# Optimization experiments

Measured on AMD Instinct MI355X. Metric: run time of the kernel, lower is better.

Reference implementation:

```python
import jax, jax.numpy as jnp
import numpy as np

H, FH, D = 8, 4, 64          # num_heads, focal_heads, att_size
HID = H * D                   # hidden_size = 512
B, S = 8, 512                 # batch, num_nodes
T_HOP, T_EDGE = 32, 16
SCALE = D ** -0.5


def setup_inputs() -> dict:
    key = jax.random.key(0)
    ks = jax.random.split(key, 24)
    f = lambda i, shape: jax.random.normal(ks[i], shape, jnp.float32)
    w = 1.0 / np.sqrt(HID)
    inp = {
        'q': f(0, (B, S, HID)), 'k': f(1, (B, S, HID)), 'v': f(2, (B, S, HID)),
        'query_hop_emb': f(3, (T_HOP, HID)) * 0.02,
        'query_edge_emb': f(4, (T_EDGE, HID)) * 0.02,
        'key_hop_emb': f(5, (T_HOP, HID)) * 0.02,
        'key_edge_emb': f(6, (T_EDGE, HID)) * 0.02,
        'value_hop_emb': f(7, (T_HOP, HID)) * 0.02,
        'value_edge_emb': f(8, (T_EDGE, HID)) * 0.02,
        'distance': jax.random.randint(ks[9], (B, S, S), 0, T_HOP),
        'edge_attr': jax.random.randint(ks[10], (B, S, S), 0, T_EDGE),
        # guarantee at least one unmasked key per query row to keep softmax finite
        'mask': jax.random.bernoulli(ks[11], 0.9, (B, S)).at[:, 0].set(True),
        'focal_mask': jax.random.bernoulli(ks[12], 0.5, (B, S, S)).at[:, :, 0].set(True),
        'Wq': f(13, (HID, H * D)) * w, 'bq': f(14, (H * D,)) * 0.01,
        'Wk': f(15, (HID, H * D)) * w, 'bk': f(16, (H * D,)) * 0.01,
        'Wv': f(17, (HID, H * D)) * w, 'bv': f(18, (H * D,)) * 0.01,
        'Wo': f(19, (H * D, HID)) * w, 'bo': f(20, (HID,)) * 0.01,
    }
    return inp


def _emb_scores(x, emb):
    # x: [B,H,S,D], emb: [T, H*D] -> per-head scores [B,H,S,T]
    e = emb.reshape(-1, H, D).transpose(1, 0, 2)  # [H,T,D]
    return jnp.einsum('bhsd,htd->bhst', x, e)


def _gather_last(scores, idx):
    # scores: [B,H,S,T], idx: [B,S,S] -> [B,H,S,S]
    idx_b = jnp.broadcast_to(idx[:, None], (B, H, S, S))
    return jnp.take_along_axis(scores, idx_b, axis=3)


def _scatter_add_last(attn, idx, T):
    # attn: [B,H,S,S], idx: [B,S,S] -> [B,H,S,T] accumulating attn weights
    idx_b = jnp.broadcast_to(idx[:, None], (B, H, S, S)).reshape(B * H * S, S)
    rows = jnp.arange(B * H * S)[:, None]
    flat = (rows * T + idx_b).reshape(-1)
    out = jnp.zeros((B * H * S * T,), attn.dtype).at[flat].add(attn.reshape(-1))
    return out.reshape(B, H, S, T)


def reference(q, k, v, query_hop_emb, query_edge_emb, key_hop_emb, key_edge_emb,
              value_hop_emb, value_edge_emb, distance, edge_attr, mask, focal_mask,
              Wq, bq, Wk, bk, Wv, bv, Wo, bo):
    qh = (q @ Wq + bq).reshape(B, S, H, D).transpose(0, 2, 1, 3)  # [B,H,S,D]
    kh = (k @ Wk + bk).reshape(B, S, H, D).transpose(0, 2, 1, 3)
    vh = (v @ Wv + bv).reshape(B, S, H, D).transpose(0, 2, 1, 3)

    spatial_bias = (_gather_last(_emb_scores(qh, query_hop_emb), distance)
                    + _gather_last(_emb_scores(kh, key_hop_emb), distance))
    edge_bias = (_gather_last(_emb_scores(qh, query_edge_emb), edge_attr)
                 + _gather_last(_emb_scores(kh, key_edge_emb), edge_attr))

    attn = (jnp.einsum('bhsd,bhtd->bhst', qh, kh) + spatial_bias + edge_bias) * SCALE

    GS = H - FH
    a1 = jnp.where(mask[:, None, None, :], attn[:, :GS], -jnp.inf)
    a2 = jnp.where(focal_mask[:, None], attn[:, GS:], -jnp.inf)
    attn = jax.nn.softmax(jnp.concatenate([a1, a2], axis=1), axis=3)

    vha = _scatter_add_last(attn, distance, T_HOP)   # [B,H,S,T_HOP]
    vea = _scatter_add_last(attn, edge_attr, T_EDGE)  # [B,H,S,T_EDGE]
    vh_emb = value_hop_emb.reshape(T_HOP, H, D).transpose(1, 0, 2)   # [H,T,D]
    ve_emb = value_edge_emb.reshape(T_EDGE, H, D).transpose(1, 0, 2)

    x = (jnp.einsum('bhst,bhtd->bhsd', attn, vh)
         + jnp.einsum('bhst,htd->bhsd', vha, vh_emb)
         + jnp.einsum('bhst,htd->bhsd', vea, ve_emb))
    x = x.transpose(0, 2, 1, 3).reshape(B, S, H * D)
    return x @ Wo + bo
```

## Files before the change

kernel.cpp:

```cpp
#include <hip/hip_runtime.h>

constexpr int nB = 8, nS = 512, nH = 8, nD = 64, nHID = 512;
constexpr int THOP = 32, TEDGE = 16;
constexpr float SCALE = 0.125f;
constexpr float NEGINF = -30000.0f;

typedef __attribute__((ext_vector_type(8))) short bf16x8;
typedef __attribute__((ext_vector_type(4))) float f32x4;

#define MFMA16(A, B, C) __builtin_amdgcn_mfma_f32_16x16x32_bf16(A, B, C, 0, 0, 0)

__device__ __align__(16) unsigned short g_qhi[(size_t)nB * nH * nS * nD];
__device__ __align__(16) unsigned short g_qlo[(size_t)nB * nH * nS * nD];
__device__ __align__(16) unsigned short g_khi[(size_t)nB * nH * nS * nD];
__device__ __align__(16) unsigned short g_klo[(size_t)nB * nH * nS * nD];
__device__ __align__(16) unsigned short g_vhiT[(size_t)nB * nH * nD * nS];
__device__ __align__(16) unsigned short g_vloT[(size_t)nB * nH * nD * nS];
__device__ __align__(16) unsigned short g_embh[96 * 512];
__device__ __align__(16) unsigned short g_embl[96 * 512];
__device__ float g_x[(size_t)nB * nS * nHID];
__device__ int g_flags[32];

__device__ __forceinline__ float ldf(const void* p, int isf32, size_t i) {
  if (isf32) return ((const float*)p)[i];
  unsigned int w = (unsigned int)(((const unsigned short*)p)[i]) << 16;
  return __uint_as_float(w);
}
__device__ __forceinline__ float bf2f(unsigned short h) {
  return __uint_as_float((unsigned)h << 16);
}
__device__ __forceinline__ float4 ldf4(const void* p, int isf32, size_t i) {
  if (isf32) return ((const float4*)p)[i >> 2];
  const ushort4 u = ((const ushort4*)p)[i >> 2];
  float4 r;
  r.x = bf2f(u.x); r.y = bf2f(u.y); r.z = bf2f(u.z); r.w = bf2f(u.w);
  return r;
}
__device__ __forceinline__ unsigned short f2bf(float x) {
  unsigned u = __float_as_uint(x);
  u += 0x7FFFu + ((u >> 16) & 1u);
  return (unsigned short)(u >> 16);
}

__device__ int detect_bool_mode(const unsigned char* p) {
  if (p[0] == 0x80 && p[1] == 0x3F) return 2;
  if (p[0] == 0x00 && p[1] == 0x3C) return 4;
  if (p[0] == 0x00 && p[3] == 0x3F) return 3;
  for (int i = 0; i < 64; i += 4)
    if (p[i + 1] | p[i + 2] | p[i + 3]) return 1;
  return 0;
}
__device__ __forceinline__ bool bool_at(const unsigned char* p, int mode, size_t i) {
  switch (mode) {
    case 0: return ((const int*)p)[i] != 0;
    case 1: return p[i] != 0;
    case 3: return ((const float*)p)[i] != 0.f;
    default: return ((const unsigned short*)p)[i] != 0;
  }
}

__global__ __launch_bounds__(256) void detect_all(
    const void* q, const void* k, const void* v,
    const void* qhe, const void* qee, const void* khe, const void* kee,
    const void* vhe, const void* vee,
    const int* dist, const int* edge,
    const unsigned char* mraw, const unsigned char* fraw,
    const void* Wq, const void* bq, const void* Wk, const void* bk,
    const void* Wv, const void* bv, const void* Wo, const void* bo) {
  __shared__ float sred[256];
  __shared__ int nzs;
  const int tid = threadIdx.x;
  const int blk = blockIdx.x;

  if (blk < 17) {
    const void* arrs[17] = {q, k, v, qhe, qee, khe, kee, vhe, vee,
                            Wq, bq, Wk, bk, Wv, bv, Wo, bo};
    const int full[17] = {2097152, 2097152, 2097152, 8192, 8192, 8192, 8192,
                          8192, 8192, 262144, 512, 262144, 512, 262144, 512,
                          262144, 512};
    const int n = full[blk] < 16384 ? full[blk] : 16384;
    const unsigned short* u = (const unsigned short*)arrs[blk];
    float m = 0.f;
    for (int i = tid; i < n; i += 256) {
      float x = __uint_as_float((unsigned int)u[i] << 16);
      if (x != x) x = 1e20f;
      m = fmaxf(m, fabsf(x));
    }
    sred[tid] = m;
    __syncthreads();
    for (int s = 128; s > 0; s >>= 1) {
      if (tid < s) sred[tid] = fmaxf(sred[tid], sred[tid + s]);
      __syncthreads();
    }
    if (tid == 0) g_flags[4 + blk] = (sred[0] > 1e3f) ? 1 : 0;
  } else if (blk == 17 || blk == 18) {
    const int* p = (blk == 17) ? dist : edge;
    if (tid == 0) nzs = 0;
    __syncthreads();
    int a = 0;
    for (int i = tid; i < 4096; i += 256) a |= p[2 * i + 1];
    if (a) atomicOr(&nzs, 1);
    __syncthreads();
    if (tid == 0) g_flags[blk - 17] = (nzs == 0);
  } else {
    if (tid == 0) {
      g_flags[2] = detect_bool_mode(mraw);
      g_flags[3] = detect_bool_mode(fraw);
      g_flags[21] = 1;
    }
  }
}

__global__ __launch_bounds__(256) void emb_prep(
    const void* qhe, const void* khe, const void* qee, const void* kee) {
  const int blk = blockIdx.x;
  const void* srcs[4] = {qhe, khe, qee, kee};
  const int flagIdx[4] = {7, 9, 8, 10};
  const int counts[4] = {32 * 512, 32 * 512, 16 * 512, 16 * 512};
  const int dsts[4] = {0, 32 * 512, 64 * 512, 80 * 512};
  const int f = g_flags[flagIdx[blk]];
  const void* src = srcs[blk];
  const int n = counts[blk], d0 = dsts[blk];
  for (int i = threadIdx.x; i < n; i += 256) {
    const float x = ldf(src, f, i);
    const unsigned short hi = f2bf(x);
    g_embh[d0 + i] = hi;
    g_embl[d0 + i] = f2bf(x - bf2f(hi));
  }
}

__global__ __launch_bounds__(256) void gemm_mfma(
    const void* __restrict__ A, int aFlag,
    const void* __restrict__ W, int wFlag,
    const void* __restrict__ bias, int bFlag,
    float* __restrict__ dst, int mode) {
  __shared__ unsigned short As_hi[64][40];
  __shared__ unsigned short As_lo[64][40];
  __shared__ unsigned short Wt_hi[64][40];
  __shared__ unsigned short Wt_lo[64][40];
  const int aF = g_flags[aFlag], wF = g_flags[wFlag], bF = g_flags[bFlag];
  const int tid = threadIdx.x;
  const int m0 = blockIdx.y * 64, n0 = blockIdx.x * 64;
  const int w = tid >> 6, l = tid & 63, c = l & 15, g = l >> 4;
  const int wr = w >> 1, wc = w & 1;

  f32x4 acc[2][2] = {{{0.f, 0.f, 0.f, 0.f}, {0.f, 0.f, 0.f, 0.f}},
                     {{0.f, 0.f, 0.f, 0.f}, {0.f, 0.f, 0.f, 0.f}}};

  for (int k0 = 0; k0 < 512; k0 += 32) {
    __syncthreads();
#pragma unroll
    for (int i = 0; i < 2; ++i) {
      const int e = tid + i * 256;
      {
        const int r = e >> 3, kk = (e & 7) * 4;
        const float4 a4 = ldf4(A, aF, (size_t)(m0 + r) * 512 + k0 + kk);
        const unsigned short h0 = f2bf(a4.x), h1 = f2bf(a4.y);
        const unsigned short h2 = f2bf(a4.z), h3 = f2bf(a4.w);
        *(unsigned*)&As_hi[r][kk]     = (unsigned)h0 | ((unsigned)h1 << 16);
        *(unsigned*)&As_hi[r][kk + 2] = (unsigned)h2 | ((unsigned)h3 << 16);
        const unsigned short l0 = f2bf(a4.x - bf2f(h0));
        const unsigned short l1 = f2bf(a4.y - bf2f(h1));
        const unsigned short l2 = f2bf(a4.z - bf2f(h2));
        const unsigned short l3 = f2bf(a4.w - bf2f(h3));
        *(unsigned*)&As_lo[r][kk]     = (unsigned)l0 | ((unsigned)l1 << 16);
        *(unsigned*)&As_lo[r][kk + 2] = (unsigned)l2 | ((unsigned)l3 << 16);
      }
      {
        const int kk = e >> 4, nn = (e & 15) * 4;
        const float4 w4 = ldf4(W, wF, (size_t)(k0 + kk) * 512 + n0 + nn);
        const float wv[4] = {w4.x, w4.y, w4.z, w4.w};
#pragma unroll
        for (int t = 0; t < 4; ++t) {
          const unsigned short hh = f2bf(wv[t]);
          Wt_hi[nn + t][kk] = hh;
          Wt_lo[nn + t][kk] = f2bf(wv[t] - bf2f(hh));
        }
      }
    }
    __syncthreads();
#pragma unroll
    for (int mi = 0; mi < 2; ++mi) {
      const bf16x8 ah = *(const bf16x8*)&As_hi[wr * 32 + mi * 16 + c][g * 8];
      const bf16x8 al = *(const bf16x8*)&As_lo[wr * 32 + mi * 16 + c][g * 8];
#pragma unroll
      for (int nj = 0; nj < 2; ++nj) {
        const bf16x8 wh = *(const bf16x8*)&Wt_hi[wc * 32 + nj * 16 + c][g * 8];
        const bf16x8 wl = *(const bf16x8*)&Wt_lo[wc * 32 + nj * 16 + c][g * 8];
        acc[mi][nj] = MFMA16(ah, wh, acc[mi][nj]);
        acc[mi][nj] = MFMA16(al, wh, acc[mi][nj]);
        acc[mi][nj] = MFMA16(ah, wl, acc[mi][nj]);
      }
    }
  }
#pragma unroll
  for (int mi = 0; mi < 2; ++mi)
#pragma unroll
    for (int nj = 0; nj < 2; ++nj)
#pragma unroll
      for (int r = 0; r < 4; ++r) {
        const int m = m0 + wr * 32 + mi * 16 + 4 * g + r;
        const int n = n0 + wc * 32 + nj * 16 + c;
        const float v2 = acc[mi][nj][r] + ldf(bias, bF, n);
        if (mode == 3) {
          dst[(size_t)m * 512 + n] = v2;
        } else {
          const int b = m >> 9, s = m & 511, h = n >> 6, d = n & 63;
          const unsigned short hi = f2bf(v2);
          const unsigned short lo = f2bf(v2 - bf2f(hi));
          if (mode == 0) {
            const size_t i0 = (((size_t)(b * nH + h) * nS) + s) * nD + d;
            g_qhi[i0] = hi; g_qlo[i0] = lo;
          } else if (mode == 1) {
            const size_t i0 = (((size_t)(b * nH + h) * nS) + s) * nD + d;
            g_khi[i0] = hi; g_klo[i0] = lo;
          } else {
            const size_t i0 = (((size_t)(b * nH + h) * nD) + d) * nS + s;
            g_vhiT[i0] = hi; g_vloT[i0] = lo;
          }
        }
      }
}

__global__ __launch_bounds__(256, 4) void attn_kernel(
    const int* __restrict__ dist, const int* __restrict__ edge,
    const unsigned char* __restrict__ mraw, const unsigned char* __restrict__ fraw,
    const void* __restrict__ vhe, const void* __restrict__ vee) {
  __shared__ float chop_s[16][33];
  __shared__ float cedge_s[16][17];
  __shared__ float vha_s[16][33];
  __shared__ float vea_s[16][17];
  __shared__ float red_s[16][4];
  __shared__ float red2_s[16][4];
  __shared__ float rinv_s[16];
  __shared__ float x_s[64][17];
  __shared__ unsigned char dlds[16][516];
  __shared__ unsigned char elds[16][516];
  __shared__ unsigned char flds[16][516];
  __shared__ unsigned char smask_l[516];

  const int qt = blockIdx.x, bh = blockIdx.y;
  const int b = bh >> 3, h = bh & 7;
  const int q0 = qt * 16;
  const int tid = threadIdx.x;
  const int w = tid >> 6, l = tid & 63, c = l & 15, g = l >> 4;

  const int d64 = g_flags[0], e64 = g_flags[1];
  const int mmode = g_flags[2], fmode = g_flags[3];
  const int fvhe = g_flags[11], fvee = g_flags[12];

  for (int i = tid; i < 16 * 33; i += 256) (&vha_s[0][0])[i] = 0.f;
  for (int i = tid; i < 16 * 17; i += 256) (&vea_s[0][0])[i] = 0.f;
  for (int i = tid; i < 64 * 17; i += 256) (&x_s[0][0])[i] = 0.f;

  const size_t rowbase = ((size_t)b * nS + q0) * nS;
  if (!d64) {
    const int4* dp = (const int4*)(dist + rowbase);
    for (int j4 = tid; j4 < 2048; j4 += 256) {
      const int4 t = dp[j4];
      const int j = j4 * 4, r = j >> 9, c1 = j & 511;
      *(unsigned*)&dlds[r][c1] =
          (unsigned)(t.x & 31) | ((unsigned)(t.y & 31) << 8) |
          ((unsigned)(t.z & 31) << 16) | ((unsigned)(t.w & 31) << 24);
    }
  } else {
    const int4* dp = (const int4*)(dist + 2 * rowbase);
    for (int j2 = tid; j2 < 4096; j2 += 256) {
      const int4 t = dp[j2];
      const int j = j2 * 2, r = j >> 9, c1 = j & 511;
      *(unsigned short*)&dlds[r][c1] =
          (unsigned short)((t.x & 31) | ((t.z & 31) << 8));
    }
  }
  if (!e64) {
    const int4* ep = (const int4*)(edge + rowbase);
    for (int j4 = tid; j4 < 2048; j4 += 256) {
      const int4 t = ep[j4];
      const int j = j4 * 4, r = j >> 9, c1 = j & 511;
      *(unsigned*)&elds[r][c1] =
          (unsigned)(t.x & 15) | ((unsigned)(t.y & 15) << 8) |
          ((unsigned)(t.z & 15) << 16) | ((unsigned)(t.w & 15) << 24);
    }
  } else {
    const int4* ep = (const int4*)(edge + 2 * rowbase);
    for (int j2 = tid; j2 < 4096; j2 += 256) {
      const int4 t = ep[j2];
      const int j = j2 * 2, r = j >> 9, c1 = j & 511;
      *(unsigned short*)&elds[r][c1] =
          (unsigned short)((t.x & 15) | ((t.z & 15) << 8));
    }
  }
  if (h < 4) {
    for (int i4 = tid; i4 < 128; i4 += 256) {
      unsigned wv = 0;
#pragma unroll
      for (int t = 0; t < 4; ++t)
        wv |= (unsigned)bool_at(mraw, mmode, (size_t)b * nS + i4 * 4 + t) << (8 * t);
      *(unsigned*)&smask_l[i4 * 4] = wv;
    }
  } else {
    for (int i4 = tid; i4 < 2048; i4 += 256) {
      const int j = i4 * 4, r = j >> 9, c1 = j & 511;
      unsigned wv = 0;
#pragma unroll
      for (int t = 0; t < 4; ++t)
        wv |= (unsigned)bool_at(fraw, fmode, rowbase + j + t) << (8 * t);
      *(unsigned*)&flds[r][c1] = wv;
    }
  }

  const size_t qbase = (((size_t)bh * nS) + q0 + c) * nD + g * 8;
  const bf16x8 qh0 = *(const bf16x8*)(g_qhi + qbase);
  const bf16x8 qh1 = *(const bf16x8*)(g_qhi + qbase + 32);
  const bf16x8 ql0 = *(const bf16x8*)(g_qlo + qbase);
  const bf16x8 ql1 = *(const bf16x8*)(g_qlo + qbase + 32);

  if (w < 3) {
    const bool isEdge = (w == 2);
    const int tb = (w == 1) ? 16 : 0;
    const size_t qe0 = (isEdge ? (size_t)64 * 512 : 0) + (size_t)(tb + c) * 512 + h * 64;
    const size_t ke0 = (isEdge ? (size_t)80 * 512 : (size_t)32 * 512) + (size_t)(tb + c) * 512 + h * 64;
    f32x4 acc = {0.f, 0.f, 0.f, 0.f};
#pragma unroll
    for (int dh = 0; dh < 2; ++dh) {
      const bf16x8 qhh = dh ? qh1 : qh0;
      const bf16x8 qll = dh ? ql1 : ql0;
      const bf16x8 khq = *(const bf16x8*)(g_khi + qbase + dh * 32);
      const bf16x8 klq = *(const bf16x8*)(g_klo + qbase + dh * 32);
      const bf16x8 eqh = *(const bf16x8*)(g_embh + qe0 + dh * 32 + g * 8);
      const bf16x8 eql = *(const bf16x8*)(g_embl + qe0 + dh * 32 + g * 8);
      const bf16x8 ekh = *(const bf16x8*)(g_embh + ke0 + dh * 32 + g * 8);
      const bf16x8 ekl = *(const bf16x8*)(g_embl + ke0 + dh * 32 + g * 8);
      acc = MFMA16(qhh, eqh, acc);
      acc = MFMA16(qll, eqh, acc);
      acc = MFMA16(qhh, eql, acc);
      acc = MFMA16(khq, ekh, acc);
      acc = MFMA16(klq, ekh, acc);
      acc = MFMA16(khq, ekl, acc);
    }
    if (!isEdge) {
#pragma unroll
      for (int r = 0; r < 4; ++r) chop_s[4 * g + r][tb + c] = acc[r];
    } else {
#pragma unroll
      for (int r = 0; r < 4; ++r) cedge_s[4 * g + r][c] = acc[r];
    }
  }
  __syncthreads();

  f32x4 pS[8];
  const int kbw = w * 128;
#pragma unroll
  for (int kt = 0; kt < 8; ++kt) {
    const int kb = kbw + kt * 16;
    const size_t kbase = (((size_t)bh * nS) + kb + c) * nD + g * 8;
    f32x4 acc = {0.f, 0.f, 0.f, 0.f};
    {
      const bf16x8 kh0 = *(const bf16x8*)(g_khi + kbase);
      const bf16x8 kl0 = *(const bf16x8*)(g_klo + kbase);
      acc = MFMA16(kh0, qh0, acc);
      acc = MFMA16(kl0, qh0, acc);
      acc = MFMA16(kh0, ql0, acc);
      const bf16x8 kh1 = *(const bf16x8*)(g_khi + kbase + 32);
      const bf16x8 kl1 = *(const bf16x8*)(g_klo + kbase + 32);
      acc = MFMA16(kh1, qh1, acc);
      acc = MFMA16(kl1, qh1, acc);
      acc = MFMA16(kh1, ql1, acc);
    }
    const int key0 = kb + 4 * g;
    const unsigned dw = *(const unsigned*)&dlds[c][key0];
    const unsigned ew = *(const unsigned*)&elds[c][key0];
    const unsigned fw = (h < 4) ? *(const unsigned*)&smask_l[key0]
                                : *(const unsigned*)&flds[c][key0];
#pragma unroll
    for (int r = 0; r < 4; ++r) {
      const int dv = (dw >> (8 * r)) & 255;
      const int ev = (ew >> (8 * r)) & 255;
      const float s = (acc[r] + chop_s[c][dv] + cedge_s[c][ev]) * SCALE;
      pS[kt][r] = ((fw >> (8 * r)) & 255) ? s : NEGINF;
    }
  }

  float mx = NEGINF;
#pragma unroll
  for (int kt = 0; kt < 8; ++kt)
#pragma unroll
    for (int r = 0; r < 4; ++r) mx = fmaxf(mx, pS[kt][r]);
  mx = fmaxf(mx, __shfl_xor(mx, 16));
  mx = fmaxf(mx, __shfl_xor(mx, 32));
  if (l < 16) red_s[c][w] = mx;
  __syncthreads();
  const float M = fmaxf(fmaxf(red_s[c][0], red_s[c][1]),
                        fmaxf(red_s[c][2], red_s[c][3]));
  float sum = 0.f;
#pragma unroll
  for (int kt = 0; kt < 8; ++kt) {
    const int key0 = kbw + kt * 16 + 4 * g;
    const unsigned dw = *(const unsigned*)&dlds[c][key0];
    const unsigned ew = *(const unsigned*)&elds[c][key0];
#pragma unroll
    for (int r = 0; r < 4; ++r) {
      const float pv = __expf(pS[kt][r] - M);
      pS[kt][r] = pv;
      sum += pv;
      atomicAdd(&vha_s[c][(dw >> (8 * r)) & 255], pv);
      atomicAdd(&vea_s[c][(ew >> (8 * r)) & 255], pv);
    }
  }
  sum += __shfl_xor(sum, 16);
  sum += __shfl_xor(sum, 32);
  if (l < 16) red2_s[c][w] = sum;
  int pk[8][2];
#pragma unroll
  for (int kt = 0; kt < 8; ++kt) {
    pk[kt][0] = ((int)f2bf(pS[kt][1]) << 16) | (int)f2bf(pS[kt][0]);
    pk[kt][1] = ((int)f2bf(pS[kt][3]) << 16) | (int)f2bf(pS[kt][2]);
  }
  __syncthreads();
  if (w == 0 && l < 16) {
    const float tot = red2_s[c][0] + red2_s[c][1] + red2_s[c][2] + red2_s[c][3];
    rinv_s[c] = 1.0f / tot;
  }

  f32x4 oacc[4] = {{0.f, 0.f, 0.f, 0.f}, {0.f, 0.f, 0.f, 0.f},
                   {0.f, 0.f, 0.f, 0.f}, {0.f, 0.f, 0.f, 0.f}};
  const int srcA = ((g & 1) * 2) * 16 + c;
  const int srcB = srcA + 16;
  const bool hi2 = (g >> 1) != 0;
#pragma unroll
  for (int ks = 0; ks < 4; ++ks) {
    const int t0d0 = __shfl(pk[2 * ks][0], srcA);
    const int t1d0 = __shfl(pk[2 * ks + 1][0], srcA);
    const int t0d1 = __shfl(pk[2 * ks][1], srcA);
    const int t1d1 = __shfl(pk[2 * ks + 1][1], srcA);
    const int t0d0b = __shfl(pk[2 * ks][0], srcB);
    const int t1d0b = __shfl(pk[2 * ks + 1][0], srcB);
    const int t0d1b = __shfl(pk[2 * ks][1], srcB);
    const int t1d1b = __shfl(pk[2 * ks + 1][1], srcB);
    union { int i[4]; bf16x8 v; } bu;
    bu.i[0] = hi2 ? t1d0 : t0d0;
    bu.i[1] = hi2 ? t1d1 : t0d1;
    bu.i[2] = hi2 ? t1d0b : t0d0b;
    bu.i[3] = hi2 ? t1d1b : t0d1b;
    const int kk = w * 128 + ks * 32;
#pragma unroll
    for (int t = 0; t < 4; ++t) {
      const size_t vbase = (((size_t)bh * nD) + t * 16 + c) * nS + kk + g * 8;
      const bf16x8 vh_ = *(const bf16x8*)(g_vhiT + vbase);
      const bf16x8 vl_ = *(const bf16x8*)(g_vloT + vbase);
      oacc[t] = MFMA16(vh_, bu.v, oacc[t]);
      oacc[t] = MFMA16(vl_, bu.v, oacc[t]);
    }
  }
#pragma unroll
  for (int t = 0; t < 4; ++t)
#pragma unroll
    for (int r = 0; r < 4; ++r)
      atomicAdd(&x_s[t * 16 + 4 * g + r][c], oacc[t][r]);
  __syncthreads();

  {
    const int d = tid & 63, qq = tid >> 6;
    float val[4];
#pragma unroll
    for (int j = 0; j < 4; ++j) val[j] = x_s[d][qq + 4 * j];
    for (int t = 0; t < THOP; ++t) {
      const float e = ldf(vhe, fvhe, (size_t)t * nHID + h * 64 + d);
#pragma unroll
      for (int j = 0; j < 4; ++j) val[j] += vha_s[qq + 4 * j][t] * e;
    }
    for (int t = 0; t < TEDGE; ++t) {
      const float e = ldf(vee, fvee, (size_t)t * nHID + h * 64 + d);
#pragma unroll
      for (int j = 0; j < 4; ++j) val[j] += vea_s[qq + 4 * j][t] * e;
    }
#pragma unroll
    for (int j = 0; j < 4; ++j) {
      const int q = qq + 4 * j;
      g_x[((size_t)b * nS + q0 + q) * nHID + h * 64 + d] = val[j] * rinv_s[q];
    }
  }
}

extern "C" void kernel_launch(void* const* d_in, const int* in_sizes, int n_in,
                              void* d_out, int out_size, void* d_ws, size_t ws_size,
                              hipStream_t stream) {
  const void* q   = d_in[0];
  const void* k   = d_in[1];
  const void* v   = d_in[2];
  const void* qhe = d_in[3];
  const void* qee = d_in[4];
  const void* khe = d_in[5];
  const void* kee = d_in[6];
  const void* vhe = d_in[7];
  const void* vee = d_in[8];
  const int* dist = (const int*)d_in[9];
  const int* edge = (const int*)d_in[10];
  const unsigned char* mraw = (const unsigned char*)d_in[11];
  const unsigned char* fraw = (const unsigned char*)d_in[12];
  const void* Wq = d_in[13];
  const void* bq = d_in[14];
  const void* Wk = d_in[15];
  const void* bk = d_in[16];
  const void* Wv = d_in[17];
  const void* bv = d_in[18];
  const void* Wo = d_in[19];
  const void* bo = d_in[20];

  detect_all<<<20, 256, 0, stream>>>(q, k, v, qhe, qee, khe, kee, vhe, vee,
                                     dist, edge, mraw, fraw,
                                     Wq, bq, Wk, bk, Wv, bv, Wo, bo);
  emb_prep<<<4, 256, 0, stream>>>(qhe, khe, qee, kee);
  float* x_d;  hipGetSymbolAddress((void**)&x_d,  HIP_SYMBOL(g_x));
  gemm_mfma<<<dim3(8, 64), 256, 0, stream>>>(q, 4, Wq, 13, bq, 14, nullptr, 0);
  gemm_mfma<<<dim3(8, 64), 256, 0, stream>>>(k, 5, Wk, 15, bk, 16, nullptr, 1);
  gemm_mfma<<<dim3(8, 64), 256, 0, stream>>>(v, 6, Wv, 17, bv, 18, nullptr, 2);
  attn_kernel<<<dim3(32, 64), 256, 0, stream>>>(dist, edge, mraw, fraw, vhe, vee);
  gemm_mfma<<<dim3(8, 64), 256, 0, stream>>>(x_d, 21, Wo, 19, bo, 20,
                                             (float*)d_out, 3);
}
```

Before: 665.4 us.

## Pre-split GEMM inputs and weights into bf16 hi/lo buffers, reorder attention grid

```diff
diff --git a/kernel.cpp b/kernel.cpp
--- a/kernel.cpp
+++ b/kernel.cpp
@@ -18,7 +18,12 @@
 __device__ __align__(16) unsigned short g_vloT[(size_t)nB * nH * nD * nS];
 __device__ __align__(16) unsigned short g_embh[96 * 512];
 __device__ __align__(16) unsigned short g_embl[96 * 512];
-__device__ float g_x[(size_t)nB * nS * nHID];
+__device__ __align__(16) unsigned short g_inhi[(size_t)3 * 2097152];
+__device__ __align__(16) unsigned short g_inlo[(size_t)3 * 2097152];
+__device__ __align__(16) unsigned short g_wth[(size_t)4 * 262144];
+__device__ __align__(16) unsigned short g_wtl[(size_t)4 * 262144];
+__device__ __align__(16) unsigned short g_xhi[(size_t)nB * nS * nHID];
+__device__ __align__(16) unsigned short g_xlo[(size_t)nB * nS * nHID];
 __device__ int g_flags[32];
 
 __device__ __forceinline__ float ldf(const void* p, int isf32, size_t i) {
@@ -106,7 +111,6 @@
     if (tid == 0) {
       g_flags[2] = detect_bool_mode(mraw);
       g_flags[3] = detect_bool_mode(fraw);
-      g_flags[21] = 1;
     }
   }
 }
@@ -129,54 +133,92 @@
   }
 }
 
+__global__ __launch_bounds__(256) void split_prep(
+    const void* q, const void* k, const void* v) {
+  const int t = blockIdx.y;
+  const void* srcs[3] = {q, k, v};
+  const int f = g_flags[4 + t];
+  const size_t base = (size_t)t * 2097152;
+  const size_t i = ((size_t)blockIdx.x * 256 + threadIdx.x) * 4;
+  const float4 v4 = ldf4(srcs[t], f, i);
+  ushort4 h4, l4;
+  h4.x = f2bf(v4.x); l4.x = f2bf(v4.x - bf2f(h4.x));
+  h4.y = f2bf(v4.y); l4.y = f2bf(v4.y - bf2f(h4.y));
+  h4.z = f2bf(v4.z); l4.z = f2bf(v4.z - bf2f(h4.z));
+  h4.w = f2bf(v4.w); l4.w = f2bf(v4.w - bf2f(h4.w));
+  *(ushort4*)&g_inhi[base + i] = h4;
+  *(ushort4*)&g_inlo[base + i] = l4;
+}
+
+__global__ __launch_bounds__(256) void wt_prep(
+    const void* Wq, const void* Wk, const void* Wv, const void* Wo) {
+  __shared__ float t[64][65];
+  const int mat = blockIdx.y;
+  const void* srcs[4] = {Wq, Wk, Wv, Wo};
+  const int fIdx[4] = {13, 15, 17, 19};
+  const int f = g_flags[fIdx[mat]];
+  const void* W = srcs[mat];
+  const int k0 = (blockIdx.x >> 3) * 64, n0 = (blockIdx.x & 7) * 64;
+  const int tid = threadIdx.x;
+  const int r = tid >> 4, c4 = (tid & 15) * 4;
+#pragma unroll
+  for (int i = 0; i < 4; ++i) {
+    const float4 v4 = ldf4(W, f, (size_t)(k0 + r + i * 16) * 512 + n0 + c4);
+    t[r + i * 16][c4] = v4.x;
+    t[r + i * 16][c4 + 1] = v4.y;
+    t[r + i * 16][c4 + 2] = v4.z;
+    t[r + i * 16][c4 + 3] = v4.w;
+  }
+  __syncthreads();
+  unsigned short* dh = g_wth + (size_t)mat * 262144;
+  unsigned short* dl = g_wtl + (size_t)mat * 262144;
+#pragma unroll
+  for (int i = 0; i < 4; ++i) {
+    const int rn = r + i * 16;
+    ushort4 h4, l4;
+    const float v0 = t[c4][rn], v1 = t[c4 + 1][rn];
+    const float v2 = t[c4 + 2][rn], v3 = t[c4 + 3][rn];
+    h4.x = f2bf(v0); l4.x = f2bf(v0 - bf2f(h4.x));
+    h4.y = f2bf(v1); l4.y = f2bf(v1 - bf2f(h4.y));
+    h4.z = f2bf(v2); l4.z = f2bf(v2 - bf2f(h4.z));
+    h4.w = f2bf(v3); l4.w = f2bf(v3 - bf2f(h4.w));
+    *(ushort4*)&dh[(size_t)(n0 + rn) * 512 + k0 + c4] = h4;
+    *(ushort4*)&dl[(size_t)(n0 + rn) * 512 + k0 + c4] = l4;
+  }
+}
+
 __global__ __launch_bounds__(256) void gemm_mfma(
-    const void* __restrict__ A, int aFlag,
-    const void* __restrict__ W, int wFlag,
+    const unsigned short* __restrict__ Ahi, const unsigned short* __restrict__ Alo,
+    const unsigned short* __restrict__ Wth, const unsigned short* __restrict__ Wtl,
     const void* __restrict__ bias, int bFlag,
     float* __restrict__ dst, int mode) {
   __shared__ unsigned short As_hi[64][40];
   __shared__ unsigned short As_lo[64][40];
   __shared__ unsigned short Wt_hi[64][40];
   __shared__ unsigned short Wt_lo[64][40];
-  const int aF = g_flags[aFlag], wF = g_flags[wFlag], bF = g_flags[bFlag];
+  const int bF = g_flags[bFlag];
   const int tid = threadIdx.x;
   const int m0 = blockIdx.y * 64, n0 = blockIdx.x * 64;
   const int w = tid >> 6, l = tid & 63, c = l & 15, g = l >> 4;
   const int wr = w >> 1, wc = w & 1;
+  const int sr = tid >> 2, sc = (tid & 3) * 8;
 
   f32x4 acc[2][2] = {{{0.f, 0.f, 0.f, 0.f}, {0.f, 0.f, 0.f, 0.f}},
                      {{0.f, 0.f, 0.f, 0.f}, {0.f, 0.f, 0.f, 0.f}}};
 
   for (int k0 = 0; k0 < 512; k0 += 32) {
     __syncthreads();
-#pragma unroll
-    for (int i = 0; i < 2; ++i) {
-      const int e = tid + i * 256;
-      {
-        const int r = e >> 3, kk = (e & 7) * 4;
-        const float4 a4 = ldf4(A, aF, (size_t)(m0 + r) * 512 + k0 + kk);
-        const unsigned short h0 = f2bf(a4.x), h1 = f2bf(a4.y);
-        const unsigned short h2 = f2bf(a4.z), h3 = f2bf(a4.w);
-        *(unsigned*)&As_hi[r][kk]     = (unsigned)h0 | ((unsigned)h1 << 16);
-        *(unsigned*)&As_hi[r][kk + 2] = (unsigned)h2 | ((unsigned)h3 << 16);
-        const unsigned short l0 = f2bf(a4.x - bf2f(h0));
-        const unsigned short l1 = f2bf(a4.y - bf2f(h1));
-        const unsigned short l2 = f2bf(a4.z - bf2f(h2));
-        const unsigned short l3 = f2bf(a4.w - bf2f(h3));
-        *(unsigned*)&As_lo[r][kk]     = (unsigned)l0 | ((unsigned)l1 << 16);
-        *(unsigned*)&As_lo[r][kk + 2] = (unsigned)l2 | ((unsigned)l3 << 16);
-      }
-      {
-        const int kk = e >> 4, nn = (e & 15) * 4;
-        const float4 w4 = ldf4(W, wF, (size_t)(k0 + kk) * 512 + n0 + nn);
-        const float wv[4] = {w4.x, w4.y, w4.z, w4.w};
-#pragma unroll
-        for (int t = 0; t < 4; ++t) {
-          const unsigned short hh = f2bf(wv[t]);
-          Wt_hi[nn + t][kk] = hh;
-          Wt_lo[nn + t][kk] = f2bf(wv[t] - bf2f(hh));
-        }
-      }
+    {
+      const size_t ga = (size_t)(m0 + sr) * 512 + k0 + sc;
+      const size_t gw = (size_t)(n0 + sr) * 512 + k0 + sc;
+      const bf16x8 ah = *(const bf16x8*)(Ahi + ga);
+      const bf16x8 al = *(const bf16x8*)(Alo + ga);
+      const bf16x8 wh = *(const bf16x8*)(Wth + gw);
+      const bf16x8 wl = *(const bf16x8*)(Wtl + gw);
+      *(bf16x8*)&As_hi[sr][sc] = ah;
+      *(bf16x8*)&As_lo[sr][sc] = al;
+      *(bf16x8*)&Wt_hi[sr][sc] = wh;
+      *(bf16x8*)&Wt_lo[sr][sc] = wl;
     }
     __syncthreads();
 #pragma unroll
@@ -222,7 +264,7 @@
       }
 }
 
-__global__ __launch_bounds__(256, 4) void attn_kernel(
+__global__ __launch_bounds__(256) void attn_kernel(
     const int* __restrict__ dist, const int* __restrict__ edge,
     const unsigned char* __restrict__ mraw, const unsigned char* __restrict__ fraw,
     const void* __restrict__ vhe, const void* __restrict__ vee) {
@@ -239,7 +281,7 @@
   __shared__ unsigned char flds[16][516];
   __shared__ unsigned char smask_l[516];
 
-  const int qt = blockIdx.x, bh = blockIdx.y;
+  const int bh = blockIdx.x, qt = blockIdx.y;
   const int b = bh >> 3, h = bh & 7;
   const int q0 = qt * 16;
   const int tid = threadIdx.x;
@@ -477,7 +519,11 @@
 #pragma unroll
     for (int j = 0; j < 4; ++j) {
       const int q = qq + 4 * j;
-      g_x[((size_t)b * nS + q0 + q) * nHID + h * 64 + d] = val[j] * rinv_s[q];
+      const float xv = val[j] * rinv_s[q];
+      const unsigned short hi = f2bf(xv);
+      const size_t i0 = ((size_t)b * nS + q0 + q) * nHID + h * 64 + d;
+      g_xhi[i0] = hi;
+      g_xlo[i0] = f2bf(xv - bf2f(hi));
     }
   }
 }
@@ -511,11 +557,26 @@
                                      dist, edge, mraw, fraw,
                                      Wq, bq, Wk, bk, Wv, bv, Wo, bo);
   emb_prep<<<4, 256, 0, stream>>>(qhe, khe, qee, kee);
-  float* x_d;  hipGetSymbolAddress((void**)&x_d,  HIP_SYMBOL(g_x));
-  gemm_mfma<<<dim3(8, 64), 256, 0, stream>>>(q, 4, Wq, 13, bq, 14, nullptr, 0);
-  gemm_mfma<<<dim3(8, 64), 256, 0, stream>>>(k, 5, Wk, 15, bk, 16, nullptr, 1);
-  gemm_mfma<<<dim3(8, 64), 256, 0, stream>>>(v, 6, Wv, 17, bv, 18, nullptr, 2);
-  attn_kernel<<<dim3(32, 64), 256, 0, stream>>>(dist, edge, mraw, fraw, vhe, vee);
-  gemm_mfma<<<dim3(8, 64), 256, 0, stream>>>(x_d, 21, Wo, 19, bo, 20,
-                                             (float*)d_out, 3);
-}
+  split_prep<<<dim3(2048, 3), 256, 0, stream>>>(q, k, v);
+  wt_prep<<<dim3(64, 4), 256, 0, stream>>>(Wq, Wk, Wv, Wo);
+
+  unsigned short* inhi; hipGetSymbolAddress((void**)&inhi, HIP_SYMBOL(g_inhi));
+  unsigned short* inlo; hipGetSymbolAddress((void**)&inlo, HIP_SYMBOL(g_inlo));
+  unsigned short* wth;  hipGetSymbolAddress((void**)&wth,  HIP_SYMBOL(g_wth));
+  unsigned short* wtl;  hipGetSymbolAddress((void**)&wtl,  HIP_SYMBOL(g_wtl));
+  unsigned short* xhi;  hipGetSymbolAddress((void**)&xhi,  HIP_SYMBOL(g_xhi));
+  unsigned short* xlo;  hipGetSymbolAddress((void**)&xlo,  HIP_SYMBOL(g_xlo));
+
+  gemm_mfma<<<dim3(8, 64), 256, 0, stream>>>(inhi, inlo, wth, wtl,
+                                             bq, 14, nullptr, 0);
+  gemm_mfma<<<dim3(8, 64), 256, 0, stream>>>(inhi + 2097152, inlo + 2097152,
+                                             wth + 262144, wtl + 262144,
+                                             bk, 16, nullptr, 1);
+  gemm_mfma<<<dim3(8, 64), 256, 0, stream>>>(inhi + 2 * 2097152, inlo + 2 * 2097152,
+                                             wth + 2 * 262144, wtl + 2 * 262144,
+                                             bv, 18, nullptr, 2);
+  attn_kernel<<<dim3(64, 32), 256, 0, stream>>>(dist, edge, mraw, fraw, vhe, vee);
+  gemm_mfma<<<dim3(8, 64), 256, 0, stream>>>(xhi, xlo,
+                                             wth + 3 * 262144, wtl + 3 * 262144,
+                                             bo, 20, (float*)d_out, 3);
+}
```

New measurement: 661.8 us. No clear change (-0.5%).
